# Kernel optimization log

Measured on AMD Instinct MI355X. Metric: run time of the kernel, lower is better.

Reference implementation:

```python
import jax, jax.numpy as jnp
import numpy as np

N, C_IN, C_RED, H, W = 16, 256, 64, 48, 48


def conv1x1(x, w, b):
    # x: [N, Cin, H, W], w: [Cout, Cin], b: [Cout]
    return jnp.einsum('nchw,oc->nohw', x, w) + b[None, :, None, None]


def setup_inputs() -> dict:
    key = jax.random.key(0)
    ks = jax.random.split(key, 10)
    s_in = 1.0 / np.sqrt(C_IN)
    s_red = 1.0 / np.sqrt(C_RED)
    return {
        'feature_maps': jax.random.normal(ks[0], (N, C_IN, H, W), jnp.float32),
        'global_channel_output': jax.random.normal(ks[1], (N, C_IN, H, W), jnp.float32),
        'Wq': jax.random.uniform(ks[2], (C_RED, C_IN), jnp.float32, -s_in, s_in),
        'bq': jax.random.uniform(ks[3], (C_RED,), jnp.float32, -s_in, s_in),
        'Wk': jax.random.uniform(ks[4], (C_RED, C_IN), jnp.float32, -s_in, s_in),
        'bk': jax.random.uniform(ks[5], (C_RED,), jnp.float32, -s_in, s_in),
        'Wv': jax.random.uniform(ks[6], (C_RED, C_IN), jnp.float32, -s_in, s_in),
        'bv': jax.random.uniform(ks[7], (C_RED,), jnp.float32, -s_in, s_in),
        'Watt': jax.random.uniform(ks[8], (C_IN, C_RED), jnp.float32, -s_red, s_red),
        'batt': jax.random.uniform(ks[9], (C_IN,), jnp.float32, -s_red, s_red),
    }


def reference(feature_maps, global_channel_output, Wq, bq, Wk, bk, Wv, bv, Watt, batt):
    n, _, h, w = feature_maps.shape
    hw = h * w
    q = conv1x1(feature_maps, Wq, bq).reshape(n, -1, hw)   # [N, Cr, HW]
    k = conv1x1(feature_maps, Wk, bk).reshape(n, -1, hw)   # [N, Cr, HW]
    v = conv1x1(feature_maps, Wv, bv).reshape(n, -1, hw)   # [N, Cr, HW]
    # key^T @ query -> [N, HW, HW]
    qk = jnp.einsum('nci,ncj->nij', k, q)
    # global (flattened) softmax over the whole HWxHW matrix per batch element
    qk = jax.nn.softmax(qk.reshape(n, hw * hw), axis=-1).reshape(n, hw, hw)
    att = jnp.einsum('nci,nij->ncj', v, qk).reshape(n, -1, h, w)  # [N, Cr, H, W]
    att = conv1x1(att, Watt, batt)                                 # [N, Cin, H, W]
    return global_channel_output * att + global_channel_output
```

## Files before the change

### kernel.cpp

```cpp
#include <hip/hip_runtime.h>
#include <hip/hip_bf16.h>
#include <stdint.h>

#define NB   16
#define CIN  256
#define CRED 64
#define HW   2304
#define NJT_OUT 36
#define JT_ATT  128
#define NJT_ATT 18
#define NIG  4
#define NIT  9

typedef __bf16 bf16;
typedef __bf16 bf16x8 __attribute__((ext_vector_type(8)));
typedef __bf16 bf16x4 __attribute__((ext_vector_type(4)));
typedef float  f32x4  __attribute__((ext_vector_type(4)));

__global__ __launch_bounds__(256) void prep_kernel(
    const float* __restrict__ Wq, const float* __restrict__ bq,
    const float* __restrict__ Wk, const float* __restrict__ Wv,
    const float* __restrict__ Watt,
    bf16* __restrict__ Wqb, bf16* __restrict__ Wkb, bf16* __restrict__ Wvb,
    bf16* __restrict__ Wab, float* __restrict__ bqs)
{
    const float INVLN2 = 1.44269504088896f;
    int i = blockIdx.x * 256 + threadIdx.x;
    Wqb[i] = (bf16)(Wq[i] * INVLN2);
    Wkb[i] = (bf16)Wk[i];
    Wvb[i] = (bf16)Wv[i];
    Wab[i] = (bf16)Watt[i];
    if (i < CRED) bqs[i] = bq[i] * INVLN2;
}

__global__ __launch_bounds__(256) void qkv_kernel(
    const float* __restrict__ x,
    const bf16* __restrict__ Wqb, const float* __restrict__ bqs,
    const bf16* __restrict__ Wkb, const float* __restrict__ bk,
    const bf16* __restrict__ Wvb, const float* __restrict__ bv,
    bf16* __restrict__ qT, bf16* __restrict__ kT, bf16* __restrict__ v)
{
    __shared__ __align__(16) bf16 sX[32 * 264];
    const int jt = blockIdx.x, n = blockIdx.y;
    const int jbase = jt * 32;
    const int tid = threadIdx.x;
    const int lane = tid & 63, w = tid >> 6;
    const int l15 = lane & 15, q4 = lane >> 4;

    const float* xn = x + ((size_t)n * CIN) * HW + jbase;
    #pragma unroll
    for (int it = 0; it < 8; ++it) {
        int idx = tid + 256 * it;
        int c = idx >> 3, p4 = idx & 7;
        const float4 vv = *(const float4*)(xn + c * HW + p4 * 4);
        sX[(p4 * 4 + 0) * 264 + c] = (bf16)vv.x;
        sX[(p4 * 4 + 1) * 264 + c] = (bf16)vv.y;
        sX[(p4 * 4 + 2) * 264 + c] = (bf16)vv.z;
        sX[(p4 * 4 + 3) * 264 + c] = (bf16)vv.w;
    }
    __syncthreads();

    const bf16*  Ws[3] = {Wqb, Wkb, Wvb};
    const float* bs[3] = {bqs, bk, bv};
    #pragma unroll
    for (int wi = 0; wi < 3; ++wi) {
        bf16x8 a[8];
        const bf16* Wp = Ws[wi] + (w * 16 + l15) * CIN + q4 * 8;
        #pragma unroll
        for (int ks = 0; ks < 8; ++ks) a[ks] = *(const bf16x8*)(Wp + ks * 32);
        f32x4 acc[2] = {};
        #pragma unroll
        for (int nt = 0; nt < 2; ++nt) {
            #pragma unroll
            for (int ks = 0; ks < 8; ++ks) {
                bf16x8 b = *(const bf16x8*)(sX + (nt * 16 + l15) * 264 + ks * 32 + q4 * 8);
                acc[nt] = __builtin_amdgcn_mfma_f32_16x16x32_bf16(a[ks], b, acc[nt], 0, 0, 0);
            }
        }
        const int crb = w * 16 + q4 * 4;
        const float b0 = bs[wi][crb], b1 = bs[wi][crb + 1],
                    b2 = bs[wi][crb + 2], b3 = bs[wi][crb + 3];
        if (wi < 2) {
            bf16* dst = (wi == 0 ? qT : kT) + ((size_t)n * HW) * 64;
            #pragma unroll
            for (int nt = 0; nt < 2; ++nt) {
                int pos = jbase + nt * 16 + l15;
                bf16x4 pk = {(bf16)(acc[nt].x + b0), (bf16)(acc[nt].y + b1),
                             (bf16)(acc[nt].z + b2), (bf16)(acc[nt].w + b3)};
                *(bf16x4*)(dst + pos * 64 + crb) = pk;
            }
        } else {
            bf16* dst = v + ((size_t)n * CRED) * HW;
            #pragma unroll
            for (int nt = 0; nt < 2; ++nt) {
                int pos = jbase + nt * 16 + l15;
                dst[(crb + 0) * HW + pos] = (bf16)(acc[nt].x + b0);
                dst[(crb + 1) * HW + pos] = (bf16)(acc[nt].y + b1);
                dst[(crb + 2) * HW + pos] = (bf16)(acc[nt].z + b2);
                dst[(crb + 3) * HW + pos] = (bf16)(acc[nt].w + b3);
            }
        }
    }
}

__global__ __launch_bounds__(256, 4) void attn_kernel(
    const bf16* __restrict__ qT, const bf16* __restrict__ kT,
    const bf16* __restrict__ v,
    float* __restrict__ OTp, float* __restrict__ Z)
{
    __shared__ __align__(16) bf16 sK[64 * 72];
    __shared__ __align__(16) bf16 sV[64 * 72];
    __shared__ __align__(16) bf16 sP[128 * 72];
    const int jt = blockIdx.x, ig = blockIdx.y, n = blockIdx.z;
    const int jbase = jt * JT_ATT;
    const int tid = threadIdx.x;
    const int lane = tid & 63, w = tid >> 6;
    const int l15 = lane & 15, q4 = lane >> 4;

    bf16x8 qf[2][2];
    {
        const bf16* qn = qT + ((size_t)n * HW + jbase + w * 32) * 64;
        #pragma unroll
        for (int nt = 0; nt < 2; ++nt)
            #pragma unroll
            for (int ks = 0; ks < 2; ++ks)
                qf[nt][ks] = *(const bf16x8*)(qn + (nt * 16 + l15) * 64 + ks * 32 + q4 * 8);
    }

    f32x4 oacc[4][2] = {};
    float zacc = 0.f;
    const uint4* ksrc = (const uint4*)(kT + ((size_t)n * HW) * 64);
    const bf16* vbase = v + ((size_t)n * CRED) * HW;

    const int r0 = tid >> 3, c0 = tid & 7;
    const int ibase0 = ig * NIT * 64;

    uint4 kr0 = ksrc[(ibase0 + r0) * 8 + c0];
    uint4 kr1 = ksrc[(ibase0 + r0 + 32) * 8 + c0];
    uint4 vr0 = *(const uint4*)(vbase + (size_t)r0 * HW + ibase0 + c0 * 8);
    uint4 vr1 = *(const uint4*)(vbase + (size_t)(r0 + 32) * HW + ibase0 + c0 * 8);

    uint4* dk = (uint4*)sK;
    uint4* dv = (uint4*)sV;
    bf16* sPw = sP + (w * 32) * 72;

    for (int it = 0; it < NIT; ++it) {
        __syncthreads();
        dk[r0 * 9 + c0] = kr0;
        dk[(r0 + 32) * 9 + c0] = kr1;
        dv[r0 * 9 + c0] = vr0;
        dv[(r0 + 32) * 9 + c0] = vr1;
        const int nbase = ibase0 + ((it + 1 < NIT) ? (it + 1) * 64 : 0);
        kr0 = ksrc[(nbase + r0) * 8 + c0];
        kr1 = ksrc[(nbase + r0 + 32) * 8 + c0];
        vr0 = *(const uint4*)(vbase + (size_t)r0 * HW + nbase + c0 * 8);
        vr1 = *(const uint4*)(vbase + (size_t)(r0 + 32) * HW + nbase + c0 * 8);
        __syncthreads();

        #pragma unroll
        for (int is = 0; is < 4; ++is) {
            bf16x8 kf0 = *(const bf16x8*)(sK + (is * 16 + l15) * 72 + q4 * 8);
            bf16x8 kf1 = *(const bf16x8*)(sK + (is * 16 + l15) * 72 + 32 + q4 * 8);
            #pragma unroll
            for (int nt = 0; nt < 2; ++nt) {
                f32x4 accs = {};
                accs = __builtin_amdgcn_mfma_f32_16x16x32_bf16(kf0, qf[nt][0], accs, 0, 0, 0);
                accs = __builtin_amdgcn_mfma_f32_16x16x32_bf16(kf1, qf[nt][1], accs, 0, 0, 0);
                float p0 = exp2f(accs.x), p1 = exp2f(accs.y);
                float p2 = exp2f(accs.z), p3 = exp2f(accs.w);
                zacc += (p0 + p1) + (p2 + p3);
                bf16x4 pk = {(bf16)p0, (bf16)p1, (bf16)p2, (bf16)p3};
                *(bf16x4*)(sPw + (nt * 16 + l15) * 72 + is * 16 + q4 * 4) = pk;
            }
        }
        bf16x8 pb[2][2];
        #pragma unroll
        for (int nt = 0; nt < 2; ++nt) {
            pb[nt][0] = *(const bf16x8*)(sPw + (nt * 16 + l15) * 72 + q4 * 8);
            pb[nt][1] = *(const bf16x8*)(sPw + (nt * 16 + l15) * 72 + 32 + q4 * 8);
        }
        #pragma unroll
        for (int ct = 0; ct < 4; ++ct) {
            bf16x8 vf0 = *(const bf16x8*)(sV + (ct * 16 + l15) * 72 + q4 * 8);
            bf16x8 vf1 = *(const bf16x8*)(sV + (ct * 16 + l15) * 72 + 32 + q4 * 8);
            #pragma unroll
            for (int nt = 0; nt < 2; ++nt) {
                oacc[ct][nt] = __builtin_amdgcn_mfma_f32_16x16x32_bf16(vf0, pb[nt][0], oacc[ct][nt], 0, 0, 0);
                oacc[ct][nt] = __builtin_amdgcn_mfma_f32_16x16x32_bf16(vf1, pb[nt][1], oacc[ct][nt], 0, 0, 0);
            }
        }
    }
    float* OTn = OTp + (((size_t)ig * NB + n) * HW) * 64;
    #pragma unroll
    for (int ct = 0; ct < 4; ++ct)
        #pragma unroll
        for (int nt = 0; nt < 2; ++nt) {
            int pos = jbase + w * 32 + nt * 16 + l15;
            *(f32x4*)(OTn + (size_t)pos * 64 + ct * 16 + q4 * 4) = oacc[ct][nt];
        }
    #pragma unroll
    for (int off = 32; off > 0; off >>= 1) zacc += __shfl_down(zacc, off);
    if (lane == 0) atomicAdd(Z + n, zacc);
}

__global__ __launch_bounds__(256) void out_kernel(
    const float* __restrict__ OTp, const float* __restrict__ Z,
    const bf16* __restrict__ Wab, const float* __restrict__ batt,
    const float* __restrict__ g, float* __restrict__ out)
{
    __shared__ __align__(16) bf16 sO[64 * 72];
    const int jt = blockIdx.x, n = blockIdx.y;
    const int jbase = jt * 64;
    const int tid = threadIdx.x;
    const int lane = tid & 63, w = tid >> 6;
    const int l15 = lane & 15, q4 = lane >> 4;
    const float invZ = 1.0f / Z[n];

    for (int i = tid; i < 1024; i += 256) {
        int r = i >> 4, c4 = i & 15;
        const float* p = OTp + (((size_t)n * HW) + jbase + r) * 64 + c4 * 4;
        float4 s = *(const float4*)(p);
        #pragma unroll
        for (int igx = 1; igx < NIG; ++igx) {
            float4 t = *(const float4*)(p + (size_t)igx * NB * HW * 64);
            s.x += t.x; s.y += t.y; s.z += t.z; s.w += t.w;
        }
        bf16x4 pk = {(bf16)(s.x * invZ), (bf16)(s.y * invZ),
                     (bf16)(s.z * invZ), (bf16)(s.w * invZ)};
        *(bf16x4*)(sO + r * 72 + c4 * 4) = pk;
    }
    __syncthreads();

    bf16x8 bfr[4][2];
    #pragma unroll
    for (int nt = 0; nt < 4; ++nt)
        #pragma unroll
        for (int ks = 0; ks < 2; ++ks)
            bfr[nt][ks] = *(const bf16x8*)(sO + (nt * 16 + l15) * 72 + ks * 32 + q4 * 8);

    const float* gp = g + ((size_t)n * CIN) * HW;
    float* op = out + ((size_t)n * CIN) * HW;
    #pragma unroll
    for (int mt = 0; mt < 4; ++mt) {
        const bf16* Wp = Wab + (w * 64 + mt * 16 + l15) * 64 + q4 * 8;
        bf16x8 a0 = *(const bf16x8*)(Wp);
        bf16x8 a1 = *(const bf16x8*)(Wp + 32);
        const int co = w * 64 + mt * 16 + q4 * 4;
        const float c0 = batt[co], c1 = batt[co + 1], c2 = batt[co + 2], c3 = batt[co + 3];
        #pragma unroll
        for (int nt = 0; nt < 4; ++nt) {
            f32x4 acc = {};
            acc = __builtin_amdgcn_mfma_f32_16x16x32_bf16(a0, bfr[nt][0], acc, 0, 0, 0);
            acc = __builtin_amdgcn_mfma_f32_16x16x32_bf16(a1, bfr[nt][1], acc, 0, 0, 0);
            const int pos = jbase + nt * 16 + l15;
            const float g0 = gp[(co + 0) * HW + pos], g1 = gp[(co + 1) * HW + pos];
            const float g2 = gp[(co + 2) * HW + pos], g3 = gp[(co + 3) * HW + pos];
            op[(co + 0) * HW + pos] = g0 * (acc.x + c0 + 1.0f);
            op[(co + 1) * HW + pos] = g1 * (acc.y + c1 + 1.0f);
            op[(co + 2) * HW + pos] = g2 * (acc.z + c2 + 1.0f);
            op[(co + 3) * HW + pos] = g3 * (acc.w + c3 + 1.0f);
        }
    }
}

extern "C" void kernel_launch(void* const* d_in, const int* in_sizes, int n_in,
                              void* d_out, int out_size, void* d_ws, size_t ws_size,
                              hipStream_t stream) {
    const float* x    = (const float*)d_in[0];
    const float* g    = (const float*)d_in[1];
    const float* Wq   = (const float*)d_in[2];
    const float* bq   = (const float*)d_in[3];
    const float* Wk   = (const float*)d_in[4];
    const float* bk   = (const float*)d_in[5];
    const float* Wv   = (const float*)d_in[6];
    const float* bv   = (const float*)d_in[7];
    const float* Watt = (const float*)d_in[8];
    const float* batt = (const float*)d_in[9];
    float* out = (float*)d_out;

    char* ws = (char*)d_ws;
    const size_t qkv_sz = (size_t)NB * HW * CRED * sizeof(bf16);
    bf16*  qT  = (bf16*)(ws);
    bf16*  kT  = (bf16*)(ws + qkv_sz);
    bf16*  vv  = (bf16*)(ws + 2 * qkv_sz);
    float* OTp = (float*)(ws + 3 * qkv_sz);
    char*  w2  = ws + 3 * qkv_sz + (size_t)NIG * NB * HW * CRED * sizeof(float);
    float* Zp  = (float*)(w2);
    bf16*  Wqb = (bf16*)(w2 + 256);
    bf16*  Wkb = Wqb + CRED * CIN;
    bf16*  Wvb = Wkb + CRED * CIN;
    bf16*  Wab = Wvb + CRED * CIN;
    float* bqs = (float*)(Wab + CIN * CRED);

    hipMemsetAsync(Zp, 0, NB * sizeof(float), stream);

    dim3 blk(256);
    prep_kernel<<<dim3(64), blk, 0, stream>>>(Wq, bq, Wk, Wv, Watt, Wqb, Wkb, Wvb, Wab, bqs);
    qkv_kernel<<<dim3(HW / 32, NB), blk, 0, stream>>>(x, Wqb, bqs, Wkb, bk, Wvb, bv, qT, kT, vv);
    attn_kernel<<<dim3(NJT_ATT, NIG, NB), blk, 0, stream>>>(qT, kT, vv, OTp, Zp);
    out_kernel<<<dim3(NJT_OUT, NB), blk, 0, stream>>>(OTp, Zp, Wab, batt, g, out);
}
```

Baseline: 248.7 us.

## Double-buffer K/V tiles, keep P in registers, shrink output tiles

The attention kernel now double-buffers the K and V shared-memory tiles, so the next tile is staged after compute and each iteration needs one barrier instead of two. The softmax probabilities are packed into bf16 registers with v_cvt_pk_bf16_f32 and fed straight into the PV MFMA, which removes the sP shared-memory round trip. V is stored in shared memory with a permuted column order so that the MFMA output layout of P lines up with the B operand. The output kernel uses 32-position tiles, doubling its block count for better occupancy, at the cost of loading the attention weights twice as often.

```diff
diff --git a/kernel.cpp b/kernel.cpp
--- a/kernel.cpp
+++ b/kernel.cpp
@@ -6,7 +6,6 @@
 #define CIN  256
 #define CRED 64
 #define HW   2304
-#define NJT_OUT 36
 #define JT_ATT  128
 #define NJT_ATT 18
 #define NIG  4
@@ -108,9 +107,8 @@
     const bf16* __restrict__ v,
     float* __restrict__ OTp, float* __restrict__ Z)
 {
-    __shared__ __align__(16) bf16 sK[64 * 72];
-    __shared__ __align__(16) bf16 sV[64 * 72];
-    __shared__ __align__(16) bf16 sP[128 * 72];
+    __shared__ __align__(16) bf16 sK[2][64 * 72];
+    __shared__ __align__(16) bf16 sV[2][64 * 72];
     const int jt = blockIdx.x, ig = blockIdx.y, n = blockIdx.z;
     const int jbase = jt * JT_ATT;
     const int tid = threadIdx.x;
@@ -134,60 +132,89 @@
 
     const int r0 = tid >> 3, c0 = tid & 7;
     const int ibase0 = ig * NIT * 64;
+    const int pbase = ((c0 >> 2) & 1) * 32 + (c0 & 1) * 16 + ((c0 >> 1) & 1) * 4;
 
     uint4 kr0 = ksrc[(ibase0 + r0) * 8 + c0];
     uint4 kr1 = ksrc[(ibase0 + r0 + 32) * 8 + c0];
     uint4 vr0 = *(const uint4*)(vbase + (size_t)r0 * HW + ibase0 + c0 * 8);
     uint4 vr1 = *(const uint4*)(vbase + (size_t)(r0 + 32) * HW + ibase0 + c0 * 8);
 
-    uint4* dk = (uint4*)sK;
-    uint4* dv = (uint4*)sV;
-    bf16* sPw = sP + (w * 32) * 72;
-
-    for (int it = 0; it < NIT; ++it) {
-        __syncthreads();
+    auto stage = [&](int buf) {
+        uint4* dk = (uint4*)sK[buf];
         dk[r0 * 9 + c0] = kr0;
         dk[(r0 + 32) * 9 + c0] = kr1;
-        dv[r0 * 9 + c0] = vr0;
-        dv[(r0 + 32) * 9 + c0] = vr1;
-        const int nbase = ibase0 + ((it + 1 < NIT) ? (it + 1) * 64 : 0);
-        kr0 = ksrc[(nbase + r0) * 8 + c0];
-        kr1 = ksrc[(nbase + r0 + 32) * 8 + c0];
-        vr0 = *(const uint4*)(vbase + (size_t)r0 * HW + nbase + c0 * 8);
-        vr1 = *(const uint4*)(vbase + (size_t)(r0 + 32) * HW + nbase + c0 * 8);
-        __syncthreads();
-
+        bf16* dv0 = sV[buf] + r0 * 72 + pbase;
+        bf16* dv1 = sV[buf] + (r0 + 32) * 72 + pbase;
+        uint2 t;
+        t.x = vr0.x; t.y = vr0.y; *(uint2*)(dv0)     = t;
+        t.x = vr0.z; t.y = vr0.w; *(uint2*)(dv0 + 8) = t;
+        t.x = vr1.x; t.y = vr1.y; *(uint2*)(dv1)     = t;
+        t.x = vr1.z; t.y = vr1.w; *(uint2*)(dv1 + 8) = t;
+    };
+
+    stage(0);
+    {
+        const int nb = ibase0 + ((1 < NIT) ? 64 : 0);
+        kr0 = ksrc[(nb + r0) * 8 + c0];
+        kr1 = ksrc[(nb + r0 + 32) * 8 + c0];
+        vr0 = *(const uint4*)(vbase + (size_t)r0 * HW + nb + c0 * 8);
+        vr1 = *(const uint4*)(vbase + (size_t)(r0 + 32) * HW + nb + c0 * 8);
+    }
+    __syncthreads();
+
+    for (int it = 0; it < NIT; ++it) {
+        const int cur = it & 1;
+        const bf16* K = sK[cur];
+        const bf16* V = sV[cur];
+
+        unsigned pw[2][4][2];
         #pragma unroll
         for (int is = 0; is < 4; ++is) {
-            bf16x8 kf0 = *(const bf16x8*)(sK + (is * 16 + l15) * 72 + q4 * 8);
-            bf16x8 kf1 = *(const bf16x8*)(sK + (is * 16 + l15) * 72 + 32 + q4 * 8);
+            bf16x8 kf0 = *(const bf16x8*)(K + (is * 16 + l15) * 72 + q4 * 8);
+            bf16x8 kf1 = *(const bf16x8*)(K + (is * 16 + l15) * 72 + 32 + q4 * 8);
             #pragma unroll
             for (int nt = 0; nt < 2; ++nt) {
-                f32x4 accs = {};
-                accs = __builtin_amdgcn_mfma_f32_16x16x32_bf16(kf0, qf[nt][0], accs, 0, 0, 0);
-                accs = __builtin_amdgcn_mfma_f32_16x16x32_bf16(kf1, qf[nt][1], accs, 0, 0, 0);
-                float p0 = exp2f(accs.x), p1 = exp2f(accs.y);
-                float p2 = exp2f(accs.z), p3 = exp2f(accs.w);
+                f32x4 s = {};
+                s = __builtin_amdgcn_mfma_f32_16x16x32_bf16(kf0, qf[nt][0], s, 0, 0, 0);
+                s = __builtin_amdgcn_mfma_f32_16x16x32_bf16(kf1, qf[nt][1], s, 0, 0, 0);
+                float p0 = exp2f(s.x), p1 = exp2f(s.y);
+                float p2 = exp2f(s.z), p3 = exp2f(s.w);
                 zacc += (p0 + p1) + (p2 + p3);
-                bf16x4 pk = {(bf16)p0, (bf16)p1, (bf16)p2, (bf16)p3};
-                *(bf16x4*)(sPw + (nt * 16 + l15) * 72 + is * 16 + q4 * 4) = pk;
-            }
-        }
-        bf16x8 pb[2][2];
-        #pragma unroll
-        for (int nt = 0; nt < 2; ++nt) {
-            pb[nt][0] = *(const bf16x8*)(sPw + (nt * 16 + l15) * 72 + q4 * 8);
-            pb[nt][1] = *(const bf16x8*)(sPw + (nt * 16 + l15) * 72 + 32 + q4 * 8);
-        }
-        #pragma unroll
-        for (int ct = 0; ct < 4; ++ct) {
-            bf16x8 vf0 = *(const bf16x8*)(sV + (ct * 16 + l15) * 72 + q4 * 8);
-            bf16x8 vf1 = *(const bf16x8*)(sV + (ct * 16 + l15) * 72 + 32 + q4 * 8);
+                unsigned w0, w1;
+                asm("v_cvt_pk_bf16_f32 %0, %1, %2" : "=v"(w0) : "v"(p0), "v"(p1));
+                asm("v_cvt_pk_bf16_f32 %0, %1, %2" : "=v"(w1) : "v"(p2), "v"(p3));
+                pw[nt][is][0] = w0;
+                pw[nt][is][1] = w1;
+            }
+        }
+        #pragma unroll
+        for (int g = 0; g < 2; ++g) {
+            bf16x8 vf[4];
+            #pragma unroll
+            for (int ct = 0; ct < 4; ++ct)
+                vf[ct] = *(const bf16x8*)(V + (ct * 16 + l15) * 72 + g * 32 + q4 * 8);
             #pragma unroll
             for (int nt = 0; nt < 2; ++nt) {
-                oacc[ct][nt] = __builtin_amdgcn_mfma_f32_16x16x32_bf16(vf0, pb[nt][0], oacc[ct][nt], 0, 0, 0);
-                oacc[ct][nt] = __builtin_amdgcn_mfma_f32_16x16x32_bf16(vf1, pb[nt][1], oacc[ct][nt], 0, 0, 0);
-            }
+                union { unsigned u[4]; bf16x8 v8; } pb;
+                pb.u[0] = pw[nt][2 * g][0];
+                pb.u[1] = pw[nt][2 * g][1];
+                pb.u[2] = pw[nt][2 * g + 1][0];
+                pb.u[3] = pw[nt][2 * g + 1][1];
+                #pragma unroll
+                for (int ct = 0; ct < 4; ++ct)
+                    oacc[ct][nt] = __builtin_amdgcn_mfma_f32_16x16x32_bf16(
+                        vf[ct], pb.v8, oacc[ct][nt], 0, 0, 0);
+            }
+        }
+
+        if (it + 1 < NIT) {
+            stage(cur ^ 1);
+            const int nb = ibase0 + ((it + 2 < NIT) ? (it + 2) * 64 : 0);
+            kr0 = ksrc[(nb + r0) * 8 + c0];
+            kr1 = ksrc[(nb + r0 + 32) * 8 + c0];
+            vr0 = *(const uint4*)(vbase + (size_t)r0 * HW + nb + c0 * 8);
+            vr1 = *(const uint4*)(vbase + (size_t)(r0 + 32) * HW + nb + c0 * 8);
+            __syncthreads();
         }
     }
     float* OTn = OTp + (((size_t)ig * NB + n) * HW) * 64;
@@ -208,15 +235,17 @@
     const bf16* __restrict__ Wab, const float* __restrict__ batt,
     const float* __restrict__ g, float* __restrict__ out)
 {
-    __shared__ __align__(16) bf16 sO[64 * 72];
+    __shared__ __align__(16) bf16 sO[32 * 72];
     const int jt = blockIdx.x, n = blockIdx.y;
-    const int jbase = jt * 64;
+    const int jbase = jt * 32;
     const int tid = threadIdx.x;
     const int lane = tid & 63, w = tid >> 6;
     const int l15 = lane & 15, q4 = lane >> 4;
     const float invZ = 1.0f / Z[n];
 
-    for (int i = tid; i < 1024; i += 256) {
+    #pragma unroll
+    for (int i0 = 0; i0 < 2; ++i0) {
+        int i = tid + i0 * 256;
         int r = i >> 4, c4 = i & 15;
         const float* p = OTp + (((size_t)n * HW) + jbase + r) * 64 + c4 * 4;
         float4 s = *(const float4*)(p);
@@ -231,9 +260,9 @@
     }
     __syncthreads();
 
-    bf16x8 bfr[4][2];
-    #pragma unroll
-    for (int nt = 0; nt < 4; ++nt)
+    bf16x8 bfr[2][2];
+    #pragma unroll
+    for (int nt = 0; nt < 2; ++nt)
         #pragma unroll
         for (int ks = 0; ks < 2; ++ks)
             bfr[nt][ks] = *(const bf16x8*)(sO + (nt * 16 + l15) * 72 + ks * 32 + q4 * 8);
@@ -248,7 +277,7 @@
         const int co = w * 64 + mt * 16 + q4 * 4;
         const float c0 = batt[co], c1 = batt[co + 1], c2 = batt[co + 2], c3 = batt[co + 3];
         #pragma unroll
-        for (int nt = 0; nt < 4; ++nt) {
+        for (int nt = 0; nt < 2; ++nt) {
             f32x4 acc = {};
             acc = __builtin_amdgcn_mfma_f32_16x16x32_bf16(a0, bfr[nt][0], acc, 0, 0, 0);
             acc = __builtin_amdgcn_mfma_f32_16x16x32_bf16(a1, bfr[nt][1], acc, 0, 0, 0);
@@ -298,5 +327,5 @@
     prep_kernel<<<dim3(64), blk, 0, stream>>>(Wq, bq, Wk, Wv, Watt, Wqb, Wkb, Wvb, Wab, bqs);
     qkv_kernel<<<dim3(HW / 32, NB), blk, 0, stream>>>(x, Wqb, bqs, Wkb, bk, Wvb, bv, qT, kT, vv);
     attn_kernel<<<dim3(NJT_ATT, NIG, NB), blk, 0, stream>>>(qT, kT, vv, OTp, Zp);
-    out_kernel<<<dim3(NJT_OUT, NB), blk, 0, stream>>>(OTp, Zp, Wab, batt, g, out);
-}
+    out_kernel<<<dim3(HW / 32, NB), blk, 0, stream>>>(OTp, Zp, Wab, batt, g, out);
+}
```

New measurement: 246.7 us. About the same (-0.8%).
